# Kernel tuning notes

Measured on AMD Instinct MI355X. Metric: run time of the kernel, lower is better.

The kernel has to match this reference:

```python
import jax, jax.numpy as jnp
import numpy as np

B, N, E = 16, 10000, 160000
C_IN, C_SP, C_OUT = 32, 16, 32


def _glorot(key, shape):
    s = float(np.sqrt(6.0 / (shape[0] + shape[1])))
    return jax.random.uniform(key, shape, jnp.float32, -s, s)


def setup_inputs() -> dict:
    key = jax.random.key(0)
    ks = jax.random.split(key, 12)
    X = jax.random.normal(ks[0], (B, N, C_IN), jnp.float32)
    edge_index1 = jax.random.randint(ks[1], (2, E), 0, N)
    edge_weight1 = jax.random.uniform(ks[2], (E,), jnp.float32)
    res_n_id1 = jnp.arange(N)
    edge_index2 = jax.random.randint(ks[3], (2, E), 0, N)
    edge_weight2 = jax.random.uniform(ks[4], (E,), jnp.float32)
    res_n_id2 = jnp.arange(N)
    # conv1 params (in=C_IN, out=C_SP, edge_channels=1, concat=True)
    amp_w1 = _glorot(ks[5], (1, C_IN))            # [edge_ch, in]
    gate_w1 = _glorot(ks[6], (2 * C_IN + 1, 1))   # Linear(2*in+edge_ch, 1)
    gate_b1 = jnp.zeros((1,), jnp.float32)
    w1 = _glorot(ks[7], (2 * C_IN, C_SP))         # concat weight
    b1 = jnp.zeros((C_SP,), jnp.float32)
    # conv2 params (in=C_SP, out=C_OUT)
    amp_w2 = _glorot(ks[8], (1, C_SP))
    gate_w2 = _glorot(ks[9], (2 * C_SP + 1, 1))
    gate_b2 = jnp.zeros((1,), jnp.float32)
    w2 = _glorot(ks[10], (2 * C_SP, C_OUT))
    b2 = jnp.zeros((C_OUT,), jnp.float32)
    return dict(X=X, edge_index1=edge_index1, edge_weight1=edge_weight1, res_n_id1=res_n_id1,
                edge_index2=edge_index2, edge_weight2=edge_weight2, res_n_id2=res_n_id2,
                amp_w1=amp_w1, gate_w1=gate_w1, gate_b1=gate_b1, w1=w1, b1=b1,
                amp_w2=amp_w2, gate_w2=gate_w2, gate_b2=gate_b2, w2=w2, b2=b2)


def _sagela(x_src, x_dst, edge_index, edge_weight, amp_w, gate_w, gate_b, w, b):
    # x_src: [B, N_src, C], x_dst: [B, N_dst, C]
    src, dst = edge_index[0], edge_index[1]
    n_dst = x_dst.shape[1]
    C = x_src.shape[-1]
    x_j = x_src[:, src]                       # [B, E, C] gathered source feats
    x_i = x_dst[:, dst]                       # [B, E, C] gathered target feats
    e = edge_weight[:, None]                  # [E, 1] edge features
    # gate_linear(cat[x_i, x_j, e]) split into three matmuls (same math)
    wg_i, wg_j, wg_e = gate_w[:C], gate_w[C:2 * C], gate_w[2 * C:]
    lamb = jax.nn.sigmoid(x_i @ wg_i + x_j @ wg_j + (e @ wg_e)[None] + gate_b)  # [B, E, 1]
    amp = e @ amp_w                           # [E, C] edge amplification
    msg = amp[None, :, :] * x_j * lamb        # [B, E, C]
    # mean aggregation over incoming edges (scatter-add / count)
    aggr = jnp.zeros((x_src.shape[0], n_dst, C), msg.dtype).at[:, dst].add(msg)
    cnt = jnp.zeros((n_dst,), msg.dtype).at[dst].add(1.0)
    aggr = aggr / jnp.maximum(cnt, 1.0)[None, :, None]
    out = jnp.concatenate([x_dst, aggr], axis=-1) @ w + b  # [B, N_dst, out]
    return out


def reference(X, edge_index1, edge_weight1, res_n_id1, edge_index2, edge_weight2, res_n_id2,
              amp_w1, gate_w1, gate_b1, w1, b1, amp_w2, gate_w2, gate_b2, w2, b2):
    h = _sagela(X, X[:, res_n_id1], edge_index1, edge_weight1, amp_w1, gate_w1, gate_b1, w1, b1)
    h = jax.nn.leaky_relu(h, 0.01)
    out = _sagela(h, h[:, res_n_id2], edge_index2, edge_weight2, amp_w2, gate_w2, gate_b2, w2, b2)
    return out
```

## Files before the change

kernel.cpp:

```cpp
#include <hip/hip_runtime.h>
#include <math.h>

#define B 16
#define N 10000
#define E 160000
#define CAP 96

__device__ __forceinline__ ushort f2bf(float v) {
    uint u = __float_as_uint(v);
    u = (u + 0x7fffu + ((u >> 16) & 1u)) >> 16;
    return (ushort)u;
}
__device__ __forceinline__ float bf2f(ushort u) { return __uint_as_float(((uint)u) << 16); }
__device__ __forceinline__ float bf2f_lo(uint u) { return __uint_as_float(u << 16); }
__device__ __forceinline__ float bf2f_hi(uint u) { return __uint_as_float(u & 0xffff0000u); }
__device__ __forceinline__ float dec_ew(uint u) {
    return ((float)(u >> 14) + 0.5f) * (1.0f / 262144.0f);
}

__global__ __launch_bounds__(256)
void prep_bucket_kernel(const float* __restrict__ X,
                        const float* __restrict__ gate_w1,
                        const int* __restrict__ ei1, const float* __restrict__ ew1,
                        const int* __restrict__ ei2, const float* __restrict__ ew2,
                        const float* __restrict__ w1,
                        const float* __restrict__ w2,
                        ushort* __restrict__ xt,
                        float* __restrict__ gi, float* __restrict__ gj,
                        float* __restrict__ w1T, float* __restrict__ w2T,
                        int* __restrict__ bcount1, uint* __restrict__ bucket1,
                        int* __restrict__ bcount2, uint* __restrict__ bucket2) {
    int gtid = blockIdx.x * 256 + threadIdx.x;
    int gs = gridDim.x * 256;

    for (int t = gtid; t < 2 * E; t += gs) {
        if (t < E) {
            int d = ei1[E + t];
            int pos = atomicAdd(&bcount1[d], 1);
            if (pos < CAP) {
                uint q = (uint)(ew1[t] * 262144.0f);
                if (q > 262143u) q = 262143u;
                bucket1[d * CAP + pos] = (q << 14) | (uint)ei1[t];
            }
        } else {
            int e = t - E;
            int d = ei2[E + e];
            int pos = atomicAdd(&bcount2[d], 1);
            if (pos < CAP) {
                uint q = (uint)(ew2[e] * 262144.0f);
                if (q > 262143u) q = 262143u;
                bucket2[d * CAP + pos] = (q << 14) | (uint)ei2[e];
            }
        }
    }

    for (int t = gtid; t < N * B; t += gs) {
        int b = t / N;
        int n = t - b * N;
        int r = n * 16 + b;
        const float4* xr = (const float4*)(X + ((size_t)b * N + n) * 32);
        float pi = 0.f, pj = 0.f;
        union { uint u[16]; uint4 v4[4]; } pk;
        #pragma unroll
        for (int q = 0; q < 8; ++q) {
            float4 v = xr[q];
            pi += v.x * gate_w1[4*q]   + v.y * gate_w1[4*q+1]
                + v.z * gate_w1[4*q+2] + v.w * gate_w1[4*q+3];
            pj += v.x * gate_w1[32+4*q]   + v.y * gate_w1[32+4*q+1]
                + v.z * gate_w1[32+4*q+2] + v.w * gate_w1[32+4*q+3];
            pk.u[2*q]   = (uint)f2bf(v.x) | ((uint)f2bf(v.y) << 16);
            pk.u[2*q+1] = (uint)f2bf(v.z) | ((uint)f2bf(v.w) << 16);
        }
        uint4* dst = (uint4*)(xt + (size_t)r * 32);
        dst[0] = pk.v4[0]; dst[1] = pk.v4[1];
        dst[2] = pk.v4[2]; dst[3] = pk.v4[3];
        gi[r] = pi; gj[r] = pj;
    }

    if (gtid < 1024) {
        w1T[(gtid & 15) * 64 + (gtid >> 4)] = w1[gtid];
        w2T[(gtid & 31) * 32 + (gtid >> 5)] = w2[gtid];
    }
}

__global__ __launch_bounds__(256, 8)
void agg_dense1_kernel(const float* __restrict__ X,
                       const uint4* __restrict__ xt4,
                       const float* __restrict__ gi,
                       const float* __restrict__ gj,
                       const int* __restrict__ bcount,
                       const uint* __restrict__ bucket,
                       const float* __restrict__ gate_w,
                       const float* __restrict__ gate_b,
                       const float* __restrict__ amp_w,
                       const float* __restrict__ w1T,
                       const float* __restrict__ b1,
                       const float* __restrict__ gate_w2,
                       ushort* __restrict__ htb,
                       float* __restrict__ gi2, float* __restrict__ gj2) {
    __shared__ uint  s_eb[CAP];
    __shared__ float s_coef[CAP * 16];
    __shared__ float s_gi[16];
    __shared__ __align__(16) float s_x[16][36];
    __shared__ __align__(16) float s_feat[16][36];
    __shared__ __align__(16) float s_wmT[16 * 68];

    int n = blockIdx.x;
    int tid = threadIdx.x;

    int cnt = bcount[n];
    int deg = cnt < CAP ? cnt : CAP;
    if (tid < CAP / 4)
        ((uint4*)s_eb)[tid] = ((const uint4*)(bucket + (size_t)n * CAP))[tid];
    {
        int o = tid >> 4, k4 = tid & 15;
        *(float4*)&s_wmT[o * 68 + k4 * 4] = ((const float4*)w1T)[o * 16 + k4];
    }
    if (tid < 128) {
        int b = tid >> 3, q = tid & 7;
        *(float4*)&s_x[b][q * 4] = ((const float4*)(X + ((size_t)b * N + n) * 32))[q];
    }
    if (tid < 16) s_gi[tid] = gi[n * 16 + tid] + gate_b[0];
    __syncthreads();

    float wge = gate_w[64];
    for (int p = tid; p < deg * 16; p += 256) {
        int k = p >> 4, b = p & 15;
        uint pr = s_eb[k];
        float w = dec_ew(pr);
        float z = s_gi[b] + gj[(pr & 0x3FFFu) * 16 + b] + w * wge;
        s_coef[p] = w / (1.0f + __expf(-z));
    }
    __syncthreads();

    int wv = tid >> 6, l = tid & 63;
    int c8 = l & 3;
    int b  = 4 * wv + ((l >> 2) & 3);
    int h  = l >> 4;
    uint boff = (uint)b * 4 + c8;
    float a0 = 0.f, a1 = 0.f, a2 = 0.f, a3 = 0.f;
    float a4 = 0.f, a5 = 0.f, a6 = 0.f, a7 = 0.f;
    int k = h;
    for (; k + 4 < deg; k += 8) {
        uint p0 = s_eb[k], p1 = s_eb[k + 4];
        float c0 = s_coef[(k << 4) | b], c1 = s_coef[((k + 4) << 4) | b];
        uint4 u0 = xt4[(p0 & 0x3FFFu) * 64u + boff];
        uint4 u1 = xt4[(p1 & 0x3FFFu) * 64u + boff];
        a0 += c0 * bf2f_lo(u0.x) + c1 * bf2f_lo(u1.x);
        a1 += c0 * bf2f_hi(u0.x) + c1 * bf2f_hi(u1.x);
        a2 += c0 * bf2f_lo(u0.y) + c1 * bf2f_lo(u1.y);
        a3 += c0 * bf2f_hi(u0.y) + c1 * bf2f_hi(u1.y);
        a4 += c0 * bf2f_lo(u0.z) + c1 * bf2f_lo(u1.z);
        a5 += c0 * bf2f_hi(u0.z) + c1 * bf2f_hi(u1.z);
        a6 += c0 * bf2f_lo(u0.w) + c1 * bf2f_lo(u1.w);
        a7 += c0 * bf2f_hi(u0.w) + c1 * bf2f_hi(u1.w);
    }
    if (k < deg) {
        uint pr = s_eb[k];
        float cc = s_coef[(k << 4) | b];
        uint4 u = xt4[(pr & 0x3FFFu) * 64u + boff];
        a0 += cc * bf2f_lo(u.x); a1 += cc * bf2f_hi(u.x);
        a2 += cc * bf2f_lo(u.y); a3 += cc * bf2f_hi(u.y);
        a4 += cc * bf2f_lo(u.z); a5 += cc * bf2f_hi(u.z);
        a6 += cc * bf2f_lo(u.w); a7 += cc * bf2f_hi(u.w);
    }
    a0 += __shfl_xor(a0, 16, 64); a0 += __shfl_xor(a0, 32, 64);
    a1 += __shfl_xor(a1, 16, 64); a1 += __shfl_xor(a1, 32, 64);
    a2 += __shfl_xor(a2, 16, 64); a2 += __shfl_xor(a2, 32, 64);
    a3 += __shfl_xor(a3, 16, 64); a3 += __shfl_xor(a3, 32, 64);
    a4 += __shfl_xor(a4, 16, 64); a4 += __shfl_xor(a4, 32, 64);
    a5 += __shfl_xor(a5, 16, 64); a5 += __shfl_xor(a5, 32, 64);
    a6 += __shfl_xor(a6, 16, 64); a6 += __shfl_xor(a6, 32, 64);
    a7 += __shfl_xor(a7, 16, 64); a7 += __shfl_xor(a7, 32, 64);
    if (h == 0) {
        float inv = 1.0f / fmaxf((float)cnt, 1.0f);
        int cb = 8 * c8;
        s_feat[b][cb]     = a0 * amp_w[cb]     * inv;
        s_feat[b][cb + 1] = a1 * amp_w[cb + 1] * inv;
        s_feat[b][cb + 2] = a2 * amp_w[cb + 2] * inv;
        s_feat[b][cb + 3] = a3 * amp_w[cb + 3] * inv;
        s_feat[b][cb + 4] = a4 * amp_w[cb + 4] * inv;
        s_feat[b][cb + 5] = a5 * amp_w[cb + 5] * inv;
        s_feat[b][cb + 6] = a6 * amp_w[cb + 6] * inv;
        s_feat[b][cb + 7] = a7 * amp_w[cb + 7] * inv;
    }
    __syncthreads();

    {
        int o = tid & 15, bb = tid >> 4;
        const float4* wr4 = (const float4*)&s_wmT[o * 68];
        const float4* x4  = (const float4*)&s_x[bb][0];
        const float4* f4  = (const float4*)&s_feat[bb][0];
        float d = b1[o];
        #pragma unroll
        for (int q = 0; q < 8; ++q) {
            float4 wvv = wr4[q],    xv = x4[q];
            float4 wf = wr4[8 + q], fv = f4[q];
            d += xv.x * wvv.x + xv.y * wvv.y + xv.z * wvv.z + xv.w * wvv.w;
            d += fv.x * wf.x + fv.y * wf.y + fv.z * wf.z + fv.w * wf.w;
        }
        d = d > 0.0f ? d : 0.01f * d;
        htb[((size_t)n * 16 + bb) * 16 + o] = f2bf(d);
        float pi = d * gate_w2[o];
        float pj = d * gate_w2[16 + o];
        #pragma unroll
        for (int off = 8; off; off >>= 1) {
            pi += __shfl_xor(pi, off, 16);
            pj += __shfl_xor(pj, off, 16);
        }
        if (o == 0) { gi2[n * 16 + bb] = pi; gj2[n * 16 + bb] = pj; }
    }
}

__global__ __launch_bounds__(256, 8)
void agg_dense2_kernel(const uint4* __restrict__ htb4,
                       const float* __restrict__ gi,
                       const float* __restrict__ gj,
                       const int* __restrict__ bcount,
                       const uint* __restrict__ bucket,
                       const float* __restrict__ gate_w,
                       const float* __restrict__ gate_b,
                       const float* __restrict__ amp_w,
                       const float* __restrict__ w2T,
                       const float* __restrict__ b2,
                       float* __restrict__ out) {
    __shared__ uint  s_eb[CAP];
    __shared__ float s_coef[CAP * 16];
    __shared__ float s_gi[16];
    __shared__ __align__(16) float s_x[16][20];
    __shared__ __align__(16) float s_feat[16][20];
    __shared__ __align__(16) float s_wmT[32 * 36];

    int n = blockIdx.x;
    int tid = threadIdx.x;

    int cnt = bcount[n];
    int deg = cnt < CAP ? cnt : CAP;
    if (tid < CAP / 4)
        ((uint4*)s_eb)[tid] = ((const uint4*)(bucket + (size_t)n * CAP))[tid];
    {
        int o = tid >> 3, k4 = tid & 7;
        *(float4*)&s_wmT[o * 36 + k4 * 4] = ((const float4*)w2T)[o * 8 + k4];
    }
    if (tid < 32) {
        uint4 u = htb4[(size_t)n * 32 + tid];
        int b = tid >> 1, cb = (tid & 1) * 8;
        float4 f0, f1;
        f0.x = bf2f_lo(u.x); f0.y = bf2f_hi(u.x);
        f0.z = bf2f_lo(u.y); f0.w = bf2f_hi(u.y);
        f1.x = bf2f_lo(u.z); f1.y = bf2f_hi(u.z);
        f1.z = bf2f_lo(u.w); f1.w = bf2f_hi(u.w);
        *(float4*)&s_x[b][cb]     = f0;
        *(float4*)&s_x[b][cb + 4] = f1;
    }
    if (tid < 16) s_gi[tid] = gi[n * 16 + tid] + gate_b[0];
    __syncthreads();

    float wge = gate_w[32];
    for (int p = tid; p < deg * 16; p += 256) {
        int k = p >> 4, b = p & 15;
        uint pr = s_eb[k];
        float w = dec_ew(pr);
        float z = s_gi[b] + gj[(pr & 0x3FFFu) * 16 + b] + w * wge;
        s_coef[p] = w / (1.0f + __expf(-z));
    }
    __syncthreads();

    int wv = tid >> 6, l = tid & 63;
    int c8 = l & 1;
    int b  = 4 * wv + ((l >> 1) & 3);
    int qd = l >> 3;
    uint boff = (uint)b * 2 + c8;
    float a0 = 0.f, a1 = 0.f, a2 = 0.f, a3 = 0.f;
    float a4 = 0.f, a5 = 0.f, a6 = 0.f, a7 = 0.f;
    int k = qd;
    for (; k + 8 < deg; k += 16) {
        uint p0 = s_eb[k], p1 = s_eb[k + 8];
        float c0 = s_coef[(k << 4) | b], c1 = s_coef[((k + 8) << 4) | b];
        uint4 u0 = htb4[(p0 & 0x3FFFu) * 32u + boff];
        uint4 u1 = htb4[(p1 & 0x3FFFu) * 32u + boff];
        a0 += c0 * bf2f_lo(u0.x) + c1 * bf2f_lo(u1.x);
        a1 += c0 * bf2f_hi(u0.x) + c1 * bf2f_hi(u1.x);
        a2 += c0 * bf2f_lo(u0.y) + c1 * bf2f_lo(u1.y);
        a3 += c0 * bf2f_hi(u0.y) + c1 * bf2f_hi(u1.y);
        a4 += c0 * bf2f_lo(u0.z) + c1 * bf2f_lo(u1.z);
        a5 += c0 * bf2f_hi(u0.z) + c1 * bf2f_hi(u1.z);
        a6 += c0 * bf2f_lo(u0.w) + c1 * bf2f_lo(u1.w);
        a7 += c0 * bf2f_hi(u0.w) + c1 * bf2f_hi(u1.w);
    }
    if (k < deg) {
        uint pr = s_eb[k];
        float cc = s_coef[(k << 4) | b];
        uint4 u = htb4[(pr & 0x3FFFu) * 32u + boff];
        a0 += cc * bf2f_lo(u.x); a1 += cc * bf2f_hi(u.x);
        a2 += cc * bf2f_lo(u.y); a3 += cc * bf2f_hi(u.y);
        a4 += cc * bf2f_lo(u.z); a5 += cc * bf2f_hi(u.z);
        a6 += cc * bf2f_lo(u.w); a7 += cc * bf2f_hi(u.w);
    }
    a0 += __shfl_xor(a0, 8, 64); a0 += __shfl_xor(a0, 16, 64); a0 += __shfl_xor(a0, 32, 64);
    a1 += __shfl_xor(a1, 8, 64); a1 += __shfl_xor(a1, 16, 64); a1 += __shfl_xor(a1, 32, 64);
    a2 += __shfl_xor(a2, 8, 64); a2 += __shfl_xor(a2, 16, 64); a2 += __shfl_xor(a2, 32, 64);
    a3 += __shfl_xor(a3, 8, 64); a3 += __shfl_xor(a3, 16, 64); a3 += __shfl_xor(a3, 32, 64);
    a4 += __shfl_xor(a4, 8, 64); a4 += __shfl_xor(a4, 16, 64); a4 += __shfl_xor(a4, 32, 64);
    a5 += __shfl_xor(a5, 8, 64); a5 += __shfl_xor(a5, 16, 64); a5 += __shfl_xor(a5, 32, 64);
    a6 += __shfl_xor(a6, 8, 64); a6 += __shfl_xor(a6, 16, 64); a6 += __shfl_xor(a6, 32, 64);
    a7 += __shfl_xor(a7, 8, 64); a7 += __shfl_xor(a7, 16, 64); a7 += __shfl_xor(a7, 32, 64);
    if (qd == 0) {
        float inv = 1.0f / fmaxf((float)cnt, 1.0f);
        int cb = 8 * c8;
        s_feat[b][cb]     = a0 * amp_w[cb]     * inv;
        s_feat[b][cb + 1] = a1 * amp_w[cb + 1] * inv;
        s_feat[b][cb + 2] = a2 * amp_w[cb + 2] * inv;
        s_feat[b][cb + 3] = a3 * amp_w[cb + 3] * inv;
        s_feat[b][cb + 4] = a4 * amp_w[cb + 4] * inv;
        s_feat[b][cb + 5] = a5 * amp_w[cb + 5] * inv;
        s_feat[b][cb + 6] = a6 * amp_w[cb + 6] * inv;
        s_feat[b][cb + 7] = a7 * amp_w[cb + 7] * inv;
    }
    __syncthreads();

    {
        int o2 = tid & 15, bb = tid >> 4;
        const float4* wr0 = (const float4*)&s_wmT[(2 * o2) * 36];
        const float4* wr1 = (const float4*)&s_wmT[(2 * o2 + 1) * 36];
        const float4* x4  = (const float4*)&s_x[bb][0];
        const float4* f4  = (const float4*)&s_feat[bb][0];
        float d0 = b2[2 * o2], d1 = b2[2 * o2 + 1];
        #pragma unroll
        for (int q = 0; q < 4; ++q) {
            float4 xv = x4[q], fv = f4[q];
            float4 w0a = wr0[q], w0b = wr0[4 + q];
            float4 w1a = wr1[q], w1b = wr1[4 + q];
            d0 += xv.x * w0a.x + xv.y * w0a.y + xv.z * w0a.z + xv.w * w0a.w;
            d0 += fv.x * w0b.x + fv.y * w0b.y + fv.z * w0b.z + fv.w * w0b.w;
            d1 += xv.x * w1a.x + xv.y * w1a.y + xv.z * w1a.z + xv.w * w1a.w;
            d1 += fv.x * w1b.x + fv.y * w1b.y + fv.z * w1b.z + fv.w * w1b.w;
        }
        size_t ob = ((size_t)bb * N + n) * 32;
        float2 r; r.x = d0; r.y = d1;
        *(float2*)(out + ob + 2 * o2) = r;
    }
}

extern "C" void kernel_launch(void* const* d_in, const int* in_sizes, int n_in,
                              void* d_out, int out_size, void* d_ws, size_t ws_size,
                              hipStream_t stream) {
    const float* X       = (const float*)d_in[0];
    const int*   ei1     = (const int*)  d_in[1];
    const float* ew1     = (const float*)d_in[2];
    const int*   ei2     = (const int*)  d_in[4];
    const float* ew2     = (const float*)d_in[5];
    const float* amp_w1  = (const float*)d_in[7];
    const float* gate_w1 = (const float*)d_in[8];
    const float* gate_b1 = (const float*)d_in[9];
    const float* w1      = (const float*)d_in[10];
    const float* b1      = (const float*)d_in[11];
    const float* amp_w2  = (const float*)d_in[12];
    const float* gate_w2 = (const float*)d_in[13];
    const float* gate_b2 = (const float*)d_in[14];
    const float* w2      = (const float*)d_in[15];
    const float* b2      = (const float*)d_in[16];
    float* out = (float*)d_out;

    char* p = (char*)d_ws;
    ushort* xt     = (ushort*)p; p += (size_t)N * B * 32 * sizeof(ushort);
    ushort* htb    = (ushort*)p; p += (size_t)N * B * 16 * sizeof(ushort);
    float* gi1     = (float*)p;  p += (size_t)N * B * sizeof(float);
    float* gj1     = (float*)p;  p += (size_t)N * B * sizeof(float);
    float* gi2     = (float*)p;  p += (size_t)N * B * sizeof(float);
    float* gj2     = (float*)p;  p += (size_t)N * B * sizeof(float);
    uint*  bucket1 = (uint*)p;   p += (size_t)N * CAP * sizeof(uint);
    uint*  bucket2 = (uint*)p;   p += (size_t)N * CAP * sizeof(uint);
    int*   bcount1 = (int*)p;    p += (size_t)N * sizeof(int);
    int*   bcount2 = (int*)p;    p += (size_t)N * sizeof(int);
    float* w1T     = (float*)p;  p += 1024 * sizeof(float);
    float* w2T     = (float*)p;  p += 1024 * sizeof(float);

    hipMemsetAsync(bcount1, 0, 2 * (size_t)N * sizeof(int), stream);
    prep_bucket_kernel<<<2048, 256, 0, stream>>>(
        X, gate_w1, ei1, ew1, ei2, ew2, w1, w2, xt, gi1, gj1, w1T, w2T,
        bcount1, bucket1, bcount2, bucket2);

    agg_dense1_kernel<<<N, 256, 0, stream>>>(
        X, (const uint4*)xt, gi1, gj1, bcount1, bucket1,
        gate_w1, gate_b1, amp_w1, w1T, b1, gate_w2, htb, gi2, gj2);

    agg_dense2_kernel<<<N, 256, 0, stream>>>(
        (const uint4*)htb, gi2, gj2, bcount2, bucket2,
        gate_w2, gate_b2, amp_w2, w2T, b2, out);
}
```

Measured before the change: 199.9 us.

## Split batch dimension across blocks in both aggregation kernels

Each node is now handled by several blocks, each covering a subset of the batch: 4 batch elements per block in layer 1 (4N blocks) and 8 in layer 2 (2N blocks). Inside a block, edges are spread across the four wavefronts, and per-wave partial sums are combined in shared memory before the dense projection. This gives more blocks and more memory-level parallelism for the gather with a smaller shared-memory footprint. The cost is that the bucket, weight matrix and edge-coefficient setup are repeated once per batch group, and each gather covers a narrower slice of the row.

```diff
diff --git a/kernel.cpp b/kernel.cpp
--- a/kernel.cpp
+++ b/kernel.cpp
@@ -99,13 +99,15 @@
                        ushort* __restrict__ htb,
                        float* __restrict__ gi2, float* __restrict__ gj2) {
     __shared__ uint  s_eb[CAP];
-    __shared__ float s_coef[CAP * 16];
-    __shared__ float s_gi[16];
-    __shared__ __align__(16) float s_x[16][36];
-    __shared__ __align__(16) float s_feat[16][36];
+    __shared__ float s_coef[CAP * 4];
+    __shared__ float s_gi[4];
+    __shared__ __align__(16) float s_x[4][36];
+    __shared__ __align__(16) float s_featp[4][4][36];
     __shared__ __align__(16) float s_wmT[16 * 68];
 
-    int n = blockIdx.x;
+    int bid = blockIdx.x;
+    int bg = bid / N;
+    int n = bid - bg * N;
     int tid = threadIdx.x;
 
     int cnt = bcount[n];
@@ -116,48 +118,34 @@
         int o = tid >> 4, k4 = tid & 15;
         *(float4*)&s_wmT[o * 68 + k4 * 4] = ((const float4*)w1T)[o * 16 + k4];
     }
-    if (tid < 128) {
-        int b = tid >> 3, q = tid & 7;
-        *(float4*)&s_x[b][q * 4] = ((const float4*)(X + ((size_t)b * N + n) * 32))[q];
-    }
-    if (tid < 16) s_gi[tid] = gi[n * 16 + tid] + gate_b[0];
+    if (tid < 32) {
+        int bl = tid >> 3, q = tid & 7;
+        *(float4*)&s_x[bl][q * 4] =
+            ((const float4*)(X + ((size_t)(bg * 4 + bl) * N + n) * 32))[q];
+    }
+    if (tid < 4) s_gi[tid] = gi[n * 16 + bg * 4 + tid] + gate_b[0];
     __syncthreads();
 
     float wge = gate_w[64];
-    for (int p = tid; p < deg * 16; p += 256) {
-        int k = p >> 4, b = p & 15;
+    for (int p = tid; p < deg * 4; p += 256) {
+        int k = p >> 2, bl = p & 3;
         uint pr = s_eb[k];
         float w = dec_ew(pr);
-        float z = s_gi[b] + gj[(pr & 0x3FFFu) * 16 + b] + w * wge;
+        float z = s_gi[bl] + gj[(pr & 0x3FFFu) * 16 + bg * 4 + bl] + w * wge;
         s_coef[p] = w / (1.0f + __expf(-z));
     }
     __syncthreads();
 
     int wv = tid >> 6, l = tid & 63;
     int c8 = l & 3;
-    int b  = 4 * wv + ((l >> 2) & 3);
+    int bl = (l >> 2) & 3;
     int h  = l >> 4;
-    uint boff = (uint)b * 4 + c8;
+    uint boff = (uint)(bg * 4 + bl) * 4 + c8;
     float a0 = 0.f, a1 = 0.f, a2 = 0.f, a3 = 0.f;
     float a4 = 0.f, a5 = 0.f, a6 = 0.f, a7 = 0.f;
-    int k = h;
-    for (; k + 4 < deg; k += 8) {
-        uint p0 = s_eb[k], p1 = s_eb[k + 4];
-        float c0 = s_coef[(k << 4) | b], c1 = s_coef[((k + 4) << 4) | b];
-        uint4 u0 = xt4[(p0 & 0x3FFFu) * 64u + boff];
-        uint4 u1 = xt4[(p1 & 0x3FFFu) * 64u + boff];
-        a0 += c0 * bf2f_lo(u0.x) + c1 * bf2f_lo(u1.x);
-        a1 += c0 * bf2f_hi(u0.x) + c1 * bf2f_hi(u1.x);
-        a2 += c0 * bf2f_lo(u0.y) + c1 * bf2f_lo(u1.y);
-        a3 += c0 * bf2f_hi(u0.y) + c1 * bf2f_hi(u1.y);
-        a4 += c0 * bf2f_lo(u0.z) + c1 * bf2f_lo(u1.z);
-        a5 += c0 * bf2f_hi(u0.z) + c1 * bf2f_hi(u1.z);
-        a6 += c0 * bf2f_lo(u0.w) + c1 * bf2f_lo(u1.w);
-        a7 += c0 * bf2f_hi(u0.w) + c1 * bf2f_hi(u1.w);
-    }
-    if (k < deg) {
+    for (int k = 4 * wv + h; k < deg; k += 16) {
         uint pr = s_eb[k];
-        float cc = s_coef[(k << 4) | b];
+        float cc = s_coef[k * 4 + bl];
         uint4 u = xt4[(pr & 0x3FFFu) * 64u + boff];
         a0 += cc * bf2f_lo(u.x); a1 += cc * bf2f_hi(u.x);
         a2 += cc * bf2f_lo(u.y); a3 += cc * bf2f_hi(u.y);
@@ -175,32 +163,42 @@
     if (h == 0) {
         float inv = 1.0f / fmaxf((float)cnt, 1.0f);
         int cb = 8 * c8;
-        s_feat[b][cb]     = a0 * amp_w[cb]     * inv;
-        s_feat[b][cb + 1] = a1 * amp_w[cb + 1] * inv;
-        s_feat[b][cb + 2] = a2 * amp_w[cb + 2] * inv;
-        s_feat[b][cb + 3] = a3 * amp_w[cb + 3] * inv;
-        s_feat[b][cb + 4] = a4 * amp_w[cb + 4] * inv;
-        s_feat[b][cb + 5] = a5 * amp_w[cb + 5] * inv;
-        s_feat[b][cb + 6] = a6 * amp_w[cb + 6] * inv;
-        s_feat[b][cb + 7] = a7 * amp_w[cb + 7] * inv;
-    }
-    __syncthreads();
-
-    {
+        s_featp[wv][bl][cb]     = a0 * amp_w[cb]     * inv;
+        s_featp[wv][bl][cb + 1] = a1 * amp_w[cb + 1] * inv;
+        s_featp[wv][bl][cb + 2] = a2 * amp_w[cb + 2] * inv;
+        s_featp[wv][bl][cb + 3] = a3 * amp_w[cb + 3] * inv;
+        s_featp[wv][bl][cb + 4] = a4 * amp_w[cb + 4] * inv;
+        s_featp[wv][bl][cb + 5] = a5 * amp_w[cb + 5] * inv;
+        s_featp[wv][bl][cb + 6] = a6 * amp_w[cb + 6] * inv;
+        s_featp[wv][bl][cb + 7] = a7 * amp_w[cb + 7] * inv;
+    }
+    __syncthreads();
+
+    if (tid < 64) {
         int o = tid & 15, bb = tid >> 4;
         const float4* wr4 = (const float4*)&s_wmT[o * 68];
         const float4* x4  = (const float4*)&s_x[bb][0];
-        const float4* f4  = (const float4*)&s_feat[bb][0];
+        const float4* f0  = (const float4*)&s_featp[0][bb][0];
+        const float4* f1  = (const float4*)&s_featp[1][bb][0];
+        const float4* f2  = (const float4*)&s_featp[2][bb][0];
+        const float4* f3  = (const float4*)&s_featp[3][bb][0];
         float d = b1[o];
         #pragma unroll
         for (int q = 0; q < 8; ++q) {
             float4 wvv = wr4[q],    xv = x4[q];
-            float4 wf = wr4[8 + q], fv = f4[q];
+            float4 wf  = wr4[8 + q];
+            float4 u0 = f0[q], u1 = f1[q], u2 = f2[q], u3 = f3[q];
+            float4 fv;
+            fv.x = (u0.x + u1.x) + (u2.x + u3.x);
+            fv.y = (u0.y + u1.y) + (u2.y + u3.y);
+            fv.z = (u0.z + u1.z) + (u2.z + u3.z);
+            fv.w = (u0.w + u1.w) + (u2.w + u3.w);
             d += xv.x * wvv.x + xv.y * wvv.y + xv.z * wvv.z + xv.w * wvv.w;
             d += fv.x * wf.x + fv.y * wf.y + fv.z * wf.z + fv.w * wf.w;
         }
         d = d > 0.0f ? d : 0.01f * d;
-        htb[((size_t)n * 16 + bb) * 16 + o] = f2bf(d);
+        int b = bg * 4 + bb;
+        htb[((size_t)n * 16 + b) * 16 + o] = f2bf(d);
         float pi = d * gate_w2[o];
         float pj = d * gate_w2[16 + o];
         #pragma unroll
@@ -208,7 +206,7 @@
             pi += __shfl_xor(pi, off, 16);
             pj += __shfl_xor(pj, off, 16);
         }
-        if (o == 0) { gi2[n * 16 + bb] = pi; gj2[n * 16 + bb] = pj; }
+        if (o == 0) { gi2[n * 16 + b] = pi; gj2[n * 16 + b] = pj; }
     }
 }
 
@@ -225,13 +223,15 @@
                        const float* __restrict__ b2,
                        float* __restrict__ out) {
     __shared__ uint  s_eb[CAP];
-    __shared__ float s_coef[CAP * 16];
-    __shared__ float s_gi[16];
-    __shared__ __align__(16) float s_x[16][20];
-    __shared__ __align__(16) float s_feat[16][20];
+    __shared__ float s_coef[CAP * 8];
+    __shared__ float s_gi[8];
+    __shared__ __align__(16) float s_x[8][20];
+    __shared__ __align__(16) float s_featp[4][8][20];
     __shared__ __align__(16) float s_wmT[32 * 36];
 
-    int n = blockIdx.x;
+    int bid = blockIdx.x;
+    int bg = bid / N;
+    int n = bid - bg * N;
     int tid = threadIdx.x;
 
     int cnt = bcount[n];
@@ -242,103 +242,91 @@
         int o = tid >> 3, k4 = tid & 7;
         *(float4*)&s_wmT[o * 36 + k4 * 4] = ((const float4*)w2T)[o * 8 + k4];
     }
-    if (tid < 32) {
-        uint4 u = htb4[(size_t)n * 32 + tid];
-        int b = tid >> 1, cb = (tid & 1) * 8;
+    if (tid < 16) {
+        uint4 u = htb4[(size_t)n * 32 + bg * 16 + tid];
+        int bl = tid >> 1, cb = (tid & 1) * 8;
         float4 f0, f1;
         f0.x = bf2f_lo(u.x); f0.y = bf2f_hi(u.x);
         f0.z = bf2f_lo(u.y); f0.w = bf2f_hi(u.y);
         f1.x = bf2f_lo(u.z); f1.y = bf2f_hi(u.z);
         f1.z = bf2f_lo(u.w); f1.w = bf2f_hi(u.w);
-        *(float4*)&s_x[b][cb]     = f0;
-        *(float4*)&s_x[b][cb + 4] = f1;
-    }
-    if (tid < 16) s_gi[tid] = gi[n * 16 + tid] + gate_b[0];
+        *(float4*)&s_x[bl][cb]     = f0;
+        *(float4*)&s_x[bl][cb + 4] = f1;
+    }
+    if (tid < 8) s_gi[tid] = gi[n * 16 + bg * 8 + tid] + gate_b[0];
     __syncthreads();
 
     float wge = gate_w[32];
-    for (int p = tid; p < deg * 16; p += 256) {
-        int k = p >> 4, b = p & 15;
+    for (int p = tid; p < deg * 8; p += 256) {
+        int k = p >> 3, bl = p & 7;
         uint pr = s_eb[k];
         float w = dec_ew(pr);
-        float z = s_gi[b] + gj[(pr & 0x3FFFu) * 16 + b] + w * wge;
+        float z = s_gi[bl] + gj[(pr & 0x3FFFu) * 16 + bg * 8 + bl] + w * wge;
         s_coef[p] = w / (1.0f + __expf(-z));
     }
     __syncthreads();
 
     int wv = tid >> 6, l = tid & 63;
     int c8 = l & 1;
-    int b  = 4 * wv + ((l >> 1) & 3);
-    int qd = l >> 3;
-    uint boff = (uint)b * 2 + c8;
+    int bl = (l >> 1) & 7;
+    int h  = l >> 4;
+    uint boff = (uint)(bg * 8 + bl) * 2 + c8;
     float a0 = 0.f, a1 = 0.f, a2 = 0.f, a3 = 0.f;
     float a4 = 0.f, a5 = 0.f, a6 = 0.f, a7 = 0.f;
-    int k = qd;
-    for (; k + 8 < deg; k += 16) {
-        uint p0 = s_eb[k], p1 = s_eb[k + 8];
-        float c0 = s_coef[(k << 4) | b], c1 = s_coef[((k + 8) << 4) | b];
-        uint4 u0 = htb4[(p0 & 0x3FFFu) * 32u + boff];
-        uint4 u1 = htb4[(p1 & 0x3FFFu) * 32u + boff];
-        a0 += c0 * bf2f_lo(u0.x) + c1 * bf2f_lo(u1.x);
-        a1 += c0 * bf2f_hi(u0.x) + c1 * bf2f_hi(u1.x);
-        a2 += c0 * bf2f_lo(u0.y) + c1 * bf2f_lo(u1.y);
-        a3 += c0 * bf2f_hi(u0.y) + c1 * bf2f_hi(u1.y);
-        a4 += c0 * bf2f_lo(u0.z) + c1 * bf2f_lo(u1.z);
-        a5 += c0 * bf2f_hi(u0.z) + c1 * bf2f_hi(u1.z);
-        a6 += c0 * bf2f_lo(u0.w) + c1 * bf2f_lo(u1.w);
-        a7 += c0 * bf2f_hi(u0.w) + c1 * bf2f_hi(u1.w);
-    }
-    if (k < deg) {
+    for (int k = 4 * wv + h; k < deg; k += 16) {
         uint pr = s_eb[k];
-        float cc = s_coef[(k << 4) | b];
+        float cc = s_coef[k * 8 + bl];
         uint4 u = htb4[(pr & 0x3FFFu) * 32u + boff];
         a0 += cc * bf2f_lo(u.x); a1 += cc * bf2f_hi(u.x);
         a2 += cc * bf2f_lo(u.y); a3 += cc * bf2f_hi(u.y);
         a4 += cc * bf2f_lo(u.z); a5 += cc * bf2f_hi(u.z);
         a6 += cc * bf2f_lo(u.w); a7 += cc * bf2f_hi(u.w);
     }
-    a0 += __shfl_xor(a0, 8, 64); a0 += __shfl_xor(a0, 16, 64); a0 += __shfl_xor(a0, 32, 64);
-    a1 += __shfl_xor(a1, 8, 64); a1 += __shfl_xor(a1, 16, 64); a1 += __shfl_xor(a1, 32, 64);
-    a2 += __shfl_xor(a2, 8, 64); a2 += __shfl_xor(a2, 16, 64); a2 += __shfl_xor(a2, 32, 64);
-    a3 += __shfl_xor(a3, 8, 64); a3 += __shfl_xor(a3, 16, 64); a3 += __shfl_xor(a3, 32, 64);
-    a4 += __shfl_xor(a4, 8, 64); a4 += __shfl_xor(a4, 16, 64); a4 += __shfl_xor(a4, 32, 64);
-    a5 += __shfl_xor(a5, 8, 64); a5 += __shfl_xor(a5, 16, 64); a5 += __shfl_xor(a5, 32, 64);
-    a6 += __shfl_xor(a6, 8, 64); a6 += __shfl_xor(a6, 16, 64); a6 += __shfl_xor(a6, 32, 64);
-    a7 += __shfl_xor(a7, 8, 64); a7 += __shfl_xor(a7, 16, 64); a7 += __shfl_xor(a7, 32, 64);
-    if (qd == 0) {
+    a0 += __shfl_xor(a0, 16, 64); a0 += __shfl_xor(a0, 32, 64);
+    a1 += __shfl_xor(a1, 16, 64); a1 += __shfl_xor(a1, 32, 64);
+    a2 += __shfl_xor(a2, 16, 64); a2 += __shfl_xor(a2, 32, 64);
+    a3 += __shfl_xor(a3, 16, 64); a3 += __shfl_xor(a3, 32, 64);
+    a4 += __shfl_xor(a4, 16, 64); a4 += __shfl_xor(a4, 32, 64);
+    a5 += __shfl_xor(a5, 16, 64); a5 += __shfl_xor(a5, 32, 64);
+    a6 += __shfl_xor(a6, 16, 64); a6 += __shfl_xor(a6, 32, 64);
+    a7 += __shfl_xor(a7, 16, 64); a7 += __shfl_xor(a7, 32, 64);
+    if (h == 0) {
         float inv = 1.0f / fmaxf((float)cnt, 1.0f);
         int cb = 8 * c8;
-        s_feat[b][cb]     = a0 * amp_w[cb]     * inv;
-        s_feat[b][cb + 1] = a1 * amp_w[cb + 1] * inv;
-        s_feat[b][cb + 2] = a2 * amp_w[cb + 2] * inv;
-        s_feat[b][cb + 3] = a3 * amp_w[cb + 3] * inv;
-        s_feat[b][cb + 4] = a4 * amp_w[cb + 4] * inv;
-        s_feat[b][cb + 5] = a5 * amp_w[cb + 5] * inv;
-        s_feat[b][cb + 6] = a6 * amp_w[cb + 6] * inv;
-        s_feat[b][cb + 7] = a7 * amp_w[cb + 7] * inv;
+        s_featp[wv][bl][cb]     = a0 * amp_w[cb]     * inv;
+        s_featp[wv][bl][cb + 1] = a1 * amp_w[cb + 1] * inv;
+        s_featp[wv][bl][cb + 2] = a2 * amp_w[cb + 2] * inv;
+        s_featp[wv][bl][cb + 3] = a3 * amp_w[cb + 3] * inv;
+        s_featp[wv][bl][cb + 4] = a4 * amp_w[cb + 4] * inv;
+        s_featp[wv][bl][cb + 5] = a5 * amp_w[cb + 5] * inv;
+        s_featp[wv][bl][cb + 6] = a6 * amp_w[cb + 6] * inv;
+        s_featp[wv][bl][cb + 7] = a7 * amp_w[cb + 7] * inv;
     }
     __syncthreads();
 
     {
-        int o2 = tid & 15, bb = tid >> 4;
-        const float4* wr0 = (const float4*)&s_wmT[(2 * o2) * 36];
-        const float4* wr1 = (const float4*)&s_wmT[(2 * o2 + 1) * 36];
-        const float4* x4  = (const float4*)&s_x[bb][0];
-        const float4* f4  = (const float4*)&s_feat[bb][0];
-        float d0 = b2[2 * o2], d1 = b2[2 * o2 + 1];
+        int o = tid & 31, bb = tid >> 5;
+        const float4* wr = (const float4*)&s_wmT[o * 36];
+        const float4* x4 = (const float4*)&s_x[bb][0];
+        const float4* f0 = (const float4*)&s_featp[0][bb][0];
+        const float4* f1 = (const float4*)&s_featp[1][bb][0];
+        const float4* f2 = (const float4*)&s_featp[2][bb][0];
+        const float4* f3 = (const float4*)&s_featp[3][bb][0];
+        float d = b2[o];
         #pragma unroll
         for (int q = 0; q < 4; ++q) {
-            float4 xv = x4[q], fv = f4[q];
-            float4 w0a = wr0[q], w0b = wr0[4 + q];
-            float4 w1a = wr1[q], w1b = wr1[4 + q];
-            d0 += xv.x * w0a.x + xv.y * w0a.y + xv.z * w0a.z + xv.w * w0a.w;
-            d0 += fv.x * w0b.x + fv.y * w0b.y + fv.z * w0b.z + fv.w * w0b.w;
-            d1 += xv.x * w1a.x + xv.y * w1a.y + xv.z * w1a.z + xv.w * w1a.w;
-            d1 += fv.x * w1b.x + fv.y * w1b.y + fv.z * w1b.z + fv.w * w1b.w;
-        }
-        size_t ob = ((size_t)bb * N + n) * 32;
-        float2 r; r.x = d0; r.y = d1;
-        *(float2*)(out + ob + 2 * o2) = r;
+            float4 xv = x4[q];
+            float4 wa = wr[q], wb = wr[4 + q];
+            float4 u0 = f0[q], u1 = f1[q], u2 = f2[q], u3 = f3[q];
+            float4 fv;
+            fv.x = (u0.x + u1.x) + (u2.x + u3.x);
+            fv.y = (u0.y + u1.y) + (u2.y + u3.y);
+            fv.z = (u0.z + u1.z) + (u2.z + u3.z);
+            fv.w = (u0.w + u1.w) + (u2.w + u3.w);
+            d += xv.x * wa.x + xv.y * wa.y + xv.z * wa.z + xv.w * wa.w;
+            d += fv.x * wb.x + fv.y * wb.y + fv.z * wb.z + fv.w * wb.w;
+        }
+        out[((size_t)(bg * 8 + bb) * N + n) * 32 + o] = d;
     }
 }
 
@@ -381,11 +369,11 @@
         X, gate_w1, ei1, ew1, ei2, ew2, w1, w2, xt, gi1, gj1, w1T, w2T,
         bcount1, bucket1, bcount2, bucket2);
 
-    agg_dense1_kernel<<<N, 256, 0, stream>>>(
+    agg_dense1_kernel<<<4 * N, 256, 0, stream>>>(
         X, (const uint4*)xt, gi1, gj1, bcount1, bucket1,
         gate_w1, gate_b1, amp_w1, w1T, b1, gate_w2, htb, gi2, gj2);
 
-    agg_dense2_kernel<<<N, 256, 0, stream>>>(
+    agg_dense2_kernel<<<2 * N, 256, 0, stream>>>(
         (const uint4*)htb, gi2, gj2, bcount2, bucket2,
         gate_w2, gate_b2, amp_w2, w2T, b2, out);
 }
```

After: 252.5 us. +26.3%, slower.
